# Optimization experiments

Measured on AMD Instinct MI355X. Metric: run time of the kernel, lower is better.

Reference implementation:

```python
import jax, jax.numpy as jnp
import numpy as np

MARGIN = 0.1
CURVATURE = 1.0
EPS = 1e-5  # keep norms strictly inside the Poincare ball for arctanh
B, D = 8192, 256


def setup_inputs() -> dict:
    key = jax.random.key(0)
    k1, k2, k3 = jax.random.split(key, 3)
    # random directions with random radii in (0, 1): valid Poincare-ball points
    v = jax.random.normal(k1, (B, D), dtype=jnp.float32)
    nrm = jnp.linalg.norm(v, axis=-1, keepdims=True)
    r = jax.random.uniform(k2, (B, 1), minval=0.05, maxval=0.95, dtype=jnp.float32)
    embeddings = v / nrm * r
    # precomputed lattice comparison matrix: cmp[i,j] in {-1, 0, 1}
    # (-1: set_i < set_j, 1: set_i > set_j, 0: incomparable). Only i<j is used.
    cmp = jax.random.randint(k3, (B, B), 0, 3, dtype=jnp.int32) - 1
    return {"embeddings": embeddings, "cmp": cmp}


def reference(embeddings, cmp):
    sc = jnp.sqrt(jnp.asarray(CURVATURE, embeddings.dtype))
    # hyperbolic distance from origin: d(x, 0) = (2/sqrt(c)) * artanh(sqrt(c)*||x||)
    nrm = jnp.linalg.norm(embeddings, axis=-1)                      # [B]
    nrm = jnp.clip(nrm, 0.0, (1.0 - EPS) / sc)
    d = (2.0 / sc) * jnp.arctanh(sc * nrm)                          # [B]

    diff = d[:, None] - d[None, :]                                   # [B,B] d_i - d_j
    triu = jnp.triu(jnp.ones((B, B), dtype=bool), k=1)               # pairs i<j only
    m_lt = triu & (cmp == -1)   # ms_i < ms_j: relu(d_i - d_j + margin)
    m_gt = triu & (cmp == 1)    # ms_i > ms_j: relu(d_j - d_i + margin)

    total = (jnp.sum(jnp.where(m_lt, jax.nn.relu(diff + MARGIN), 0.0))
             + jnp.sum(jnp.where(m_gt, jax.nn.relu(-diff + MARGIN), 0.0)))
    n_pairs = jnp.sum(m_lt) + jnp.sum(m_gt)
    return jnp.where(n_pairs > 0, total / n_pairs.astype(embeddings.dtype), 0.0)
```

## Files before the change

### kernel.cpp

```cpp
#include <hip/hip_runtime.h>

constexpr int Bdim = 8192;
constexpr int Ddim = 256;
constexpr int TILE = 256;
constexpr int NT   = Bdim / TILE;
constexpr int NTRI = NT * (NT + 1) / 2;
constexpr int RCH  = 4;
constexpr int RPC  = TILE / RCH;
constexpr int RPW  = RPC / 4;
constexpr int NPART = NTRI * RCH;
constexpr float MARGIN_F = 0.1f;

__global__ __launch_bounds__(256) void k_norm(const float* __restrict__ emb,
                                              float* __restrict__ d) {
    int row  = blockIdx.x * 4 + (threadIdx.x >> 6);
    int lane = threadIdx.x & 63;
    float4 v = ((const float4*)(emb + (size_t)row * Ddim))[lane];
    float s = v.x * v.x + v.y * v.y + v.z * v.z + v.w * v.w;
#pragma unroll
    for (int off = 32; off > 0; off >>= 1) s += __shfl_down(s, off, 64);
    if (lane == 0) {
        float n = fminf(sqrtf(s), 1.0f - 1e-5f);
        d[row] = logf((1.0f + n) / (1.0f - n));
    }
}

__global__ __launch_bounds__(256) void k_pairs(const float* __restrict__ d,
                                               const int* __restrict__ cmp,
                                               double* __restrict__ psum,
                                               unsigned int* __restrict__ pcnt) {
    int rem = blockIdx.x;
    int ti = 0;
    while (rem >= NT - ti) { rem -= NT - ti; ++ti; }
    int tj = ti + rem;

    int tid  = threadIdx.x;
    int lane = tid & 63;
    int wave = tid >> 6;

    int j0 = tj * TILE + lane * 4;
    float4 dj = *(const float4*)(d + j0);

    __shared__ float dis[RPC];
    int i0 = ti * TILE + blockIdx.y * RPC;
    if (tid < RPC) dis[tid] = d[i0 + tid];
    __syncthreads();

    int rbase = wave * RPW;
    const int4* p = (const int4*)(cmp + (size_t)(i0 + rbase) * Bdim + j0);

    float s = 0.0f;
    int cnt = 0;

    if (ti == tj) {
#pragma unroll 4
        for (int r = 0; r < RPW; ++r) {
            int   i  = i0 + rbase + r;
            float di = dis[rbase + r];
            int4  c  = p[(size_t)r * (Bdim / 4)];
            {
                bool act = (c.x != 0) & (j0 + 0 > i);
                float x = fmaf((float)c.x, dj.x - di, MARGIN_F);
                s += act ? fmaxf(x, 0.0f) : 0.0f; cnt += act ? 1 : 0;
            }
            {
                bool act = (c.y != 0) & (j0 + 1 > i);
                float x = fmaf((float)c.y, dj.y - di, MARGIN_F);
                s += act ? fmaxf(x, 0.0f) : 0.0f; cnt += act ? 1 : 0;
            }
            {
                bool act = (c.z != 0) & (j0 + 2 > i);
                float x = fmaf((float)c.z, dj.z - di, MARGIN_F);
                s += act ? fmaxf(x, 0.0f) : 0.0f; cnt += act ? 1 : 0;
            }
            {
                bool act = (c.w != 0) & (j0 + 3 > i);
                float x = fmaf((float)c.w, dj.w - di, MARGIN_F);
                s += act ? fmaxf(x, 0.0f) : 0.0f; cnt += act ? 1 : 0;
            }
        }
    } else {
#pragma unroll 4
        for (int r = 0; r < RPW; ++r) {
            float di = dis[rbase + r];
            int4  c  = p[(size_t)r * (Bdim / 4)];
            {
                bool act = (c.x != 0);
                float x = fmaf((float)c.x, dj.x - di, MARGIN_F);
                s += act ? fmaxf(x, 0.0f) : 0.0f; cnt += act ? 1 : 0;
            }
            {
                bool act = (c.y != 0);
                float x = fmaf((float)c.y, dj.y - di, MARGIN_F);
                s += act ? fmaxf(x, 0.0f) : 0.0f; cnt += act ? 1 : 0;
            }
            {
                bool act = (c.z != 0);
                float x = fmaf((float)c.z, dj.z - di, MARGIN_F);
                s += act ? fmaxf(x, 0.0f) : 0.0f; cnt += act ? 1 : 0;
            }
            {
                bool act = (c.w != 0);
                float x = fmaf((float)c.w, dj.w - di, MARGIN_F);
                s += act ? fmaxf(x, 0.0f) : 0.0f; cnt += act ? 1 : 0;
            }
        }
    }

#pragma unroll
    for (int off = 32; off > 0; off >>= 1) {
        s   += __shfl_down(s, off, 64);
        cnt += __shfl_down(cnt, off, 64);
    }
    __shared__ float ws_s[4];
    __shared__ int   ws_c[4];
    if ((tid & 63) == 0) { ws_s[wave] = s; ws_c[wave] = cnt; }
    __syncthreads();
    if (tid == 0) {
        float st = ws_s[0] + ws_s[1] + ws_s[2] + ws_s[3];
        int   ct = ws_c[0] + ws_c[1] + ws_c[2] + ws_c[3];
        int slot = blockIdx.y * NTRI + blockIdx.x;
        psum[slot] = (double)st;
        pcnt[slot] = (unsigned int)ct;
    }
}

__global__ __launch_bounds__(256) void k_final(const double* __restrict__ psum,
                                               const unsigned int* __restrict__ pcnt,
                                               float* __restrict__ out) {
    int tid = threadIdx.x;
    double s = 0.0;
    unsigned long long c = 0;
    for (int idx = tid; idx < NPART; idx += 256) {
        s += psum[idx];
        c += pcnt[idx];
    }
#pragma unroll
    for (int off = 32; off > 0; off >>= 1) {
        s += __shfl_down(s, off, 64);
        c += __shfl_down(c, off, 64);
    }
    __shared__ double sd[4];
    __shared__ unsigned long long sc[4];
    int wave = tid >> 6;
    if ((tid & 63) == 0) { sd[wave] = s; sc[wave] = c; }
    __syncthreads();
    if (tid == 0) {
        double st = sd[0] + sd[1] + sd[2] + sd[3];
        unsigned long long ct = sc[0] + sc[1] + sc[2] + sc[3];
        out[0] = (ct > 0) ? (float)(st / (double)ct) : 0.0f;
    }
}

extern "C" void kernel_launch(void* const* d_in, const int* in_sizes, int n_in,
                              void* d_out, int out_size, void* d_ws, size_t ws_size,
                              hipStream_t stream) {
    const float* emb = (const float*)d_in[0];
    const int*   cmp = (const int*)d_in[1];
    float* out = (float*)d_out;

    char* ws = (char*)d_ws;
    float*        dvec = (float*)ws;
    double*       psum = (double*)(ws + 32768);
    unsigned int* pcnt = (unsigned int*)(ws + 32768 + NPART * 8);

    hipLaunchKernelGGL(k_norm, dim3(Bdim / 4), dim3(256), 0, stream, emb, dvec);
    hipLaunchKernelGGL(k_pairs, dim3(NTRI, RCH), dim3(256), 0, stream,
                       dvec, cmp, psum, pcnt);
    hipLaunchKernelGGL(k_final, dim3(1), dim3(256), 0, stream, psum, pcnt, out);
}
```

Before: 36.95 us.

## Use grid-stride persistent blocks, nontemporal cmp loads, and skip below-diagonal waves

```diff
diff --git a/kernel.cpp b/kernel.cpp
--- a/kernel.cpp
+++ b/kernel.cpp
@@ -5,11 +5,14 @@
 constexpr int TILE = 256;
 constexpr int NT   = Bdim / TILE;
 constexpr int NTRI = NT * (NT + 1) / 2;
-constexpr int RCH  = 4;
+constexpr int RCH  = 8;
 constexpr int RPC  = TILE / RCH;
 constexpr int RPW  = RPC / 4;
-constexpr int NPART = NTRI * RCH;
+constexpr int NUNIT = NTRI * RCH;
+constexpr int NBLK  = 2048;
 constexpr float MARGIN_F = 0.1f;
+
+typedef int iv4 __attribute__((ext_vector_type(4)));
 
 __global__ __launch_bounds__(256) void k_norm(const float* __restrict__ emb,
                                               float* __restrict__ d) {
@@ -29,80 +32,81 @@
                                                const int* __restrict__ cmp,
                                                double* __restrict__ psum,
                                                unsigned int* __restrict__ pcnt) {
-    int rem = blockIdx.x;
-    int ti = 0;
-    while (rem >= NT - ti) { rem -= NT - ti; ++ti; }
-    int tj = ti + rem;
-
     int tid  = threadIdx.x;
     int lane = tid & 63;
     int wave = tid >> 6;
 
-    int j0 = tj * TILE + lane * 4;
-    float4 dj = *(const float4*)(d + j0);
-
-    __shared__ float dis[RPC];
-    int i0 = ti * TILE + blockIdx.y * RPC;
-    if (tid < RPC) dis[tid] = d[i0 + tid];
-    __syncthreads();
-
-    int rbase = wave * RPW;
-    const int4* p = (const int4*)(cmp + (size_t)(i0 + rbase) * Bdim + j0);
-
     float s = 0.0f;
     int cnt = 0;
 
-    if (ti == tj) {
+    for (int u = blockIdx.x; u < NUNIT; u += NBLK) {
+        int tri   = u % NTRI;
+        int chunk = u / NTRI;
+        int rem = tri, ti = 0;
+        while (rem >= NT - ti) { rem -= NT - ti; ++ti; }
+        int tj = ti + rem;
+
+        int i0 = ti * TILE + chunk * RPC + wave * RPW;
+        int j0 = tj * TILE + lane * 4;
+        float4 dj = *(const float4*)(d + j0);
+        const iv4* p = (const iv4*)(cmp + (size_t)i0 * Bdim + j0);
+
+        if (ti == tj) {
+            if (j0 + 3 > i0) {
+#pragma unroll
+                for (int r = 0; r < RPW; ++r) {
+                    int   i  = i0 + r;
+                    float di = d[i];
+                    iv4   c  = __builtin_nontemporal_load(p);
+                    p += Bdim / 4;
+                    {
+                        bool act = (c.x != 0) & (j0 + 0 > i);
+                        float x = fmaf((float)c.x, dj.x - di, MARGIN_F);
+                        s += act ? fmaxf(x, 0.0f) : 0.0f; cnt += act ? 1 : 0;
+                    }
+                    {
+                        bool act = (c.y != 0) & (j0 + 1 > i);
+                        float x = fmaf((float)c.y, dj.y - di, MARGIN_F);
+                        s += act ? fmaxf(x, 0.0f) : 0.0f; cnt += act ? 1 : 0;
+                    }
+                    {
+                        bool act = (c.z != 0) & (j0 + 2 > i);
+                        float x = fmaf((float)c.z, dj.z - di, MARGIN_F);
+                        s += act ? fmaxf(x, 0.0f) : 0.0f; cnt += act ? 1 : 0;
+                    }
+                    {
+                        bool act = (c.w != 0) & (j0 + 3 > i);
+                        float x = fmaf((float)c.w, dj.w - di, MARGIN_F);
+                        s += act ? fmaxf(x, 0.0f) : 0.0f; cnt += act ? 1 : 0;
+                    }
+                }
+            }
+        } else {
 #pragma unroll 4
-        for (int r = 0; r < RPW; ++r) {
-            int   i  = i0 + rbase + r;
-            float di = dis[rbase + r];
-            int4  c  = p[(size_t)r * (Bdim / 4)];
-            {
-                bool act = (c.x != 0) & (j0 + 0 > i);
-                float x = fmaf((float)c.x, dj.x - di, MARGIN_F);
-                s += act ? fmaxf(x, 0.0f) : 0.0f; cnt += act ? 1 : 0;
-            }
-            {
-                bool act = (c.y != 0) & (j0 + 1 > i);
-                float x = fmaf((float)c.y, dj.y - di, MARGIN_F);
-                s += act ? fmaxf(x, 0.0f) : 0.0f; cnt += act ? 1 : 0;
-            }
-            {
-                bool act = (c.z != 0) & (j0 + 2 > i);
-                float x = fmaf((float)c.z, dj.z - di, MARGIN_F);
-                s += act ? fmaxf(x, 0.0f) : 0.0f; cnt += act ? 1 : 0;
-            }
-            {
-                bool act = (c.w != 0) & (j0 + 3 > i);
-                float x = fmaf((float)c.w, dj.w - di, MARGIN_F);
-                s += act ? fmaxf(x, 0.0f) : 0.0f; cnt += act ? 1 : 0;
-            }
-        }
-    } else {
-#pragma unroll 4
-        for (int r = 0; r < RPW; ++r) {
-            float di = dis[rbase + r];
-            int4  c  = p[(size_t)r * (Bdim / 4)];
-            {
-                bool act = (c.x != 0);
-                float x = fmaf((float)c.x, dj.x - di, MARGIN_F);
-                s += act ? fmaxf(x, 0.0f) : 0.0f; cnt += act ? 1 : 0;
-            }
-            {
-                bool act = (c.y != 0);
-                float x = fmaf((float)c.y, dj.y - di, MARGIN_F);
-                s += act ? fmaxf(x, 0.0f) : 0.0f; cnt += act ? 1 : 0;
-            }
-            {
-                bool act = (c.z != 0);
-                float x = fmaf((float)c.z, dj.z - di, MARGIN_F);
-                s += act ? fmaxf(x, 0.0f) : 0.0f; cnt += act ? 1 : 0;
-            }
-            {
-                bool act = (c.w != 0);
-                float x = fmaf((float)c.w, dj.w - di, MARGIN_F);
-                s += act ? fmaxf(x, 0.0f) : 0.0f; cnt += act ? 1 : 0;
+            for (int r = 0; r < RPW; ++r) {
+                float di = d[i0 + r];
+                iv4   c  = __builtin_nontemporal_load(p);
+                p += Bdim / 4;
+                {
+                    bool act = (c.x != 0);
+                    float x = fmaf((float)c.x, dj.x - di, MARGIN_F);
+                    s += act ? fmaxf(x, 0.0f) : 0.0f; cnt += act ? 1 : 0;
+                }
+                {
+                    bool act = (c.y != 0);
+                    float x = fmaf((float)c.y, dj.y - di, MARGIN_F);
+                    s += act ? fmaxf(x, 0.0f) : 0.0f; cnt += act ? 1 : 0;
+                }
+                {
+                    bool act = (c.z != 0);
+                    float x = fmaf((float)c.z, dj.z - di, MARGIN_F);
+                    s += act ? fmaxf(x, 0.0f) : 0.0f; cnt += act ? 1 : 0;
+                }
+                {
+                    bool act = (c.w != 0);
+                    float x = fmaf((float)c.w, dj.w - di, MARGIN_F);
+                    s += act ? fmaxf(x, 0.0f) : 0.0f; cnt += act ? 1 : 0;
+                }
             }
         }
     }
@@ -119,9 +123,8 @@
     if (tid == 0) {
         float st = ws_s[0] + ws_s[1] + ws_s[2] + ws_s[3];
         int   ct = ws_c[0] + ws_c[1] + ws_c[2] + ws_c[3];
-        int slot = blockIdx.y * NTRI + blockIdx.x;
-        psum[slot] = (double)st;
-        pcnt[slot] = (unsigned int)ct;
+        psum[blockIdx.x] = (double)st;
+        pcnt[blockIdx.x] = (unsigned int)ct;
     }
 }
 
@@ -131,7 +134,7 @@
     int tid = threadIdx.x;
     double s = 0.0;
     unsigned long long c = 0;
-    for (int idx = tid; idx < NPART; idx += 256) {
+    for (int idx = tid; idx < NBLK; idx += 256) {
         s += psum[idx];
         c += pcnt[idx];
     }
@@ -162,10 +165,10 @@
     char* ws = (char*)d_ws;
     float*        dvec = (float*)ws;
     double*       psum = (double*)(ws + 32768);
-    unsigned int* pcnt = (unsigned int*)(ws + 32768 + NPART * 8);
+    unsigned int* pcnt = (unsigned int*)(ws + 32768 + NBLK * 8);
 
     hipLaunchKernelGGL(k_norm, dim3(Bdim / 4), dim3(256), 0, stream, emb, dvec);
-    hipLaunchKernelGGL(k_pairs, dim3(NTRI, RCH), dim3(256), 0, stream,
+    hipLaunchKernelGGL(k_pairs, dim3(NBLK), dim3(256), 0, stream,
                        dvec, cmp, psum, pcnt);
     hipLaunchKernelGGL(k_final, dim3(1), dim3(256), 0, stream, psum, pcnt, out);
 }
```

Result: faster. 35.92 us (-2.8%).
